# Kernel optimization log

Measured on AMD Instinct MI355X. Metric: run time of the kernel, lower is better.

The kernel has to match this reference:

```python
import jax, jax.numpy as jnp
from jax import lax
import numpy as np

N, CIN, COUT, K, LAT, H = 8, 512, 512, 3, 512, 32
CINT = (CIN + COUT) // 2  # inter_channels
DN = ('NCHW', 'OIHW', 'NCHW')


def setup_inputs() -> dict:
    key = jax.random.key(0)
    ks = jax.random.split(key, 16)
    f = jax.random.normal
    return {
        'x': f(ks[0], (N, CIN, H, H), jnp.float32),
        'v': f(ks[1], (N, LAT), jnp.float32),
        'y': f(ks[2], (N, 3, H, H), jnp.float32),
        'noise1': f(ks[3], (N, 1, 2 * H, 2 * H), jnp.float32),
        'noise2': f(ks[4], (N, 1, 2 * H, 2 * H), jnp.float32),
        # Up_Mod_Conv: weight stored transposed -> [in, out, k, k]
        'up_w': f(ks[5], (CIN, CINT, K, K), jnp.float32) * 0.05,
        'up_b': f(ks[6], (CINT,), jnp.float32) * 0.05,
        'up_sw': f(ks[7], (LAT, CIN), jnp.float32) * 0.02,
        'up_sb': jnp.ones((CIN,), jnp.float32),
        # Modulated_Conv2d: weight [out, in, k, k]
        'c_w': f(ks[8], (COUT, CINT, K, K), jnp.float32) * 0.05,
        'c_b': f(ks[9], (COUT,), jnp.float32) * 0.05,
        'c_sw': f(ks[10], (LAT, CINT), jnp.float32) * 0.02,
        'c_sb': jnp.ones((CINT,), jnp.float32),
        # toRGB: 1x1, no demodulation
        'rgb_w': f(ks[11], (3, COUT, 1, 1), jnp.float32) * 0.05,
        'rgb_b': f(ks[12], (3,), jnp.float32) * 0.05,
        'rgb_sw': f(ks[13], (LAT, COUT), jnp.float32) * 0.02,
        'rgb_sb': jnp.ones((COUT,), jnp.float32),
        'noise_strength': jnp.full((1,), 0.1, jnp.float32),
    }


def _lrelu(x):
    return jnp.where(x > 0, x, 0.2 * x)  # LeakyReLU(0.2)


def _mod_conv(x, v, W, b, sw, sb, demod, pad):
    # Per-sample modulation s_i * W; since conv is linear this equals
    # conv(x * s) followed by per-sample/out-channel demod division.
    s = v @ sw + sb  # [N, Cin]
    out = lax.conv_general_dilated(x * s[:, :, None, None], W, (1, 1),
                                   ((pad, pad), (pad, pad)), dimension_numbers=DN)
    if demod:
        # sigma_no = sqrt(sum_{i,h,w} (s_ni * W_oihw)^2 + eps)
        sigma = jnp.sqrt(jnp.einsum('oihw,ni->no', W * W, s * s) + 1e-8)
        out = out / sigma[:, :, None, None]
    return out + b[None, :, None, None]


def _up_mod_conv(x, v, W, b, sw, sb):
    s = v @ sw + sb  # [N, Cin]
    Wt = jnp.flip(W, axis=(2, 3)).transpose(1, 0, 2, 3)  # [out, in, k, k]
    out = lax.conv_general_dilated(x * s[:, :, None, None], Wt, (1, 1),
                                   ((1, 2), (1, 2)), lhs_dilation=(2, 2),
                                   dimension_numbers=DN)
    # demod sums over in-channel dim and spatial dims of [in,out,k,k] weight
    sigma = jnp.sqrt(jnp.einsum('iohw,ni->no', W * W, s * s) + 1e-8)
    return out / sigma[:, :, None, None] + b[None, :, None, None]


def reference(x, v, y, noise1, noise2, up_w, up_b, up_sw, up_sb,
              c_w, c_b, c_sw, c_sb, rgb_w, rgb_b, rgb_sw, rgb_sb,
              noise_strength):
    h = _up_mod_conv(x, v, up_w, up_b, up_sw, up_sb)          # [N, CINT, 2H, 2H]
    h = _lrelu(h + noise_strength[0] * noise1)
    h = _mod_conv(h, v, c_w, c_b, c_sw, c_sb, True, K // 2)   # [N, COUT, 2H, 2H]
    h = _lrelu(h + noise_strength[0] * noise2)
    rgb = _lrelu(_mod_conv(h, v, rgb_w, rgb_b, rgb_sw, rgb_sb, False, 0))
    y_up = jax.image.resize(y, (y.shape[0], y.shape[1], 2 * y.shape[2], 2 * y.shape[3]),
                            method='bilinear')  # matches torch align_corners=False
    return (h, y_up + rgb)
```

## Files before the change

kernel.cpp:

```cpp
#include <hip/hip_runtime.h>
#include <hip/hip_bf16.h>

typedef unsigned short u16;
typedef u16  u16x4 __attribute__((ext_vector_type(4)));
typedef __bf16 bf16;
typedef bf16 bf16x8 __attribute__((ext_vector_type(8)));
typedef float f32x4 __attribute__((ext_vector_type(4)));

__device__ __forceinline__ float b2f(u16 u){ return __uint_as_float(((unsigned)u)<<16); }
__device__ __forceinline__ u16 f2b(float f){ bf16 h = (bf16)f; return __builtin_bit_cast(u16, h); }
__device__ __forceinline__ float lrelu(float v){ return v > 0.f ? v : 0.2f*v; }

__device__ __forceinline__ void gll16(const u16* g, u16* l){
  __builtin_amdgcn_global_load_lds(
    (const __attribute__((address_space(1))) unsigned int*)(const void*)g,
    (__attribute__((address_space(3))) unsigned int*)(void*)l, 16, 0, 0);
}
#define VMCNT0() asm volatile("s_waitcnt vmcnt(0)" ::: "memory")
#define BAR()    { asm volatile("" ::: "memory"); __builtin_amdgcn_s_barrier(); asm volatile("" ::: "memory"); }


__global__ __launch_bounds__(256) void prep_w_up(const float* __restrict__ up_w,
                                                 u16* __restrict__ Wup_t, float* __restrict__ wsq_up){
  const int t = blockIdx.x*256 + threadIdx.x;
  const int i = t & 511, o = t >> 9;
  const float* src = up_w + ((i<<9) + o)*9;
  float sq = 0.f;
  #pragma unroll
  for (int ky=0; ky<3; ++ky)
    #pragma unroll
    for (int kx=0; kx<3; ++kx){
      float w = src[ky*3+kx];
      sq += w*w;
      Wup_t[ (((2-ky)*3 + (2-kx))<<18) + (o<<9) + i ] = f2b(w);
    }
  wsq_up[(o<<9)+i] = sq;
}

__global__ __launch_bounds__(256) void prep_w_c(const float* __restrict__ c_w,
                                                u16* __restrict__ Wc_t, float* __restrict__ wsq_c){
  const int t = blockIdx.x*256 + threadIdx.x;
  const int i = t & 511, o = t >> 9;
  const float* src = c_w + ((o<<9) + i)*9;
  float sq = 0.f;
  #pragma unroll
  for (int tap=0; tap<9; ++tap){
    float w = src[tap];
    sq += w*w;
    Wc_t[ (tap<<18) + (o<<9) + i ] = f2b(w);
  }
  wsq_c[(o<<9)+i] = sq;
}

__global__ __launch_bounds__(256) void prep_s(const float* __restrict__ v,
    const float* __restrict__ up_sw, const float* __restrict__ up_sb,
    const float* __restrict__ c_sw,  const float* __restrict__ c_sb,
    const float* __restrict__ rgb_sw,const float* __restrict__ rgb_sb,
    float* __restrict__ s_up, float* __restrict__ s_c, float* __restrict__ s_rgb){
  const int t = blockIdx.x*256 + threadIdx.x;
  const int j = t & 511, n = t >> 9;
  const float* vn = v + (n<<9);
  float a=0.f, b=0.f, c=0.f;
  for (int l=0; l<512; ++l){
    float vl = vn[l];
    a += vl*up_sw[(l<<9)+j];
    b += vl*c_sw[(l<<9)+j];
    c += vl*rgb_sw[(l<<9)+j];
  }
  s_up[t] = a + up_sb[j];
  s_c[t]  = b + c_sb[j];
  s_rgb[t]= c + rgb_sb[j];
}

__global__ __launch_bounds__(256) void prep_sigma(const float* __restrict__ wsq_up, const float* __restrict__ wsq_c,
    const float* __restrict__ s_up, const float* __restrict__ s_c,
    float* __restrict__ sinv_up, float* __restrict__ sinv_c){
  const int t = blockIdx.x*256 + threadIdx.x;
  const int o = t & 511, n = t >> 9;
  const float* su = s_up + (n<<9);
  const float* sc = s_c  + (n<<9);
  const float* wu = wsq_up + (o<<9);
  const float* wc = wsq_c  + (o<<9);
  float au=0.f, ac=0.f;
  for (int l=0; l<512; ++l){
    float s1 = su[l]; au += wu[l]*s1*s1;
    float s2 = sc[l]; ac += wc[l]*s2*s2;
  }
  sinv_up[t] = 1.f/sqrtf(au + 1e-8f);
  sinv_c[t]  = 1.f/sqrtf(ac + 1e-8f);
}

__global__ __launch_bounds__(256) void fill_xp(const float* __restrict__ x,
    const float* __restrict__ s_up, u16* __restrict__ xp){
  const int t = blockIdx.x*256 + threadIdx.x;
  const int q4 = (t&7)<<2;
  const int p  = (t>>3)&31;
  const int chn= t>>8;
  const int n  = chn>>9, ch = chn&511;
  const float s = s_up[chn];
  const float4 vx = *(const float4*)&x[ (((chn<<5)+p)<<5) + q4 ];
  const int base = (((n*33 + p)*36) + q4)<<9;
  xp[base +        ch] = f2b(vx.x*s);
  xp[base +  512 + ch] = f2b(vx.y*s);
  xp[base + 1024 + ch] = f2b(vx.z*s);
  xp[base + 1536 + ch] = f2b(vx.w*s);
}

__global__ __launch_bounds__(256, 2) void up_conv_k(
    const u16* __restrict__ xp, const u16* __restrict__ Wup_t,
    const float* __restrict__ sinv_up, const float* __restrict__ up_b,
    const float* __restrict__ s_c, const float* __restrict__ noise1,
    const float* __restrict__ nstr, u16* __restrict__ h1s)
{
  __shared__ __align__(16) u16 Bp[11520];
  __shared__ __align__(16) u16 Aa[8192];
  const int bid = blockIdx.x;
  const int og = bid & 3, tile = (bid>>2)&7, cls = (bid>>5)&3, n = bid>>7;
  const int cy = cls>>1, cx = cls&1;
  const int o0 = og<<7, r0 = tile<<2;
  const int tid = threadIdx.x;
  const int lane = tid & 63, wave = tid>>6;
  const int l15 = lane & 15, l4 = lane>>4;
  const int wm = wave>>1, wn = wave&1;
  const int xsw = l15 & 7;
  const int wub = tid & ~63;

  int wtap[4], dpl[4], dql[4]; int nt=0;
  for (int a = cy?0:1; a <= (cy?2:1); a += (cy?2:1))
    for (int b = cx?0:1; b <= (cx?2:1); b += (cx?2:1)){
      wtap[nt] = a*3+b; dpl[nt] = (cy+a-1)>>1; dql[nt] = (cx+b-1)>>1; ++nt;
    }

  f32x4 acc[4][4];
  #pragma unroll
  for (int i2=0;i2<4;++i2)
    #pragma unroll
    for (int j2=0;j2<4;++j2){ f32x4 z = {0.f,0.f,0.f,0.f}; acc[i2][j2]=z; }

  #pragma unroll 1
  for (int ci=0; ci<8; ++ci){
    const int i0 = ci<<6;
    BAR();
    #pragma unroll
    for (int k=0;k<6;++k){
      const int q = (k<<8) + tid;
      if (q < 1440){
        const int cell = q>>3, pc = q&7;
        const int rowl = cell/36, col = cell - rowl*36;
        const int cl = pc ^ (col&7);
        const u16* src = xp + (((n*33 + r0 + rowl)*36 + col)<<9) + i0 + (cl<<3);
        gll16(src, Bp + (((k<<8)+wub)<<3));
      }
    }
    #pragma unroll 1
    for (int t=0; t<nt; ++t){
      const int dp = dpl[t], dq = dql[t];
      #pragma unroll
      for (int k=0;k<4;++k){
        const int q = (k<<8) + tid;
        const int o = q>>3, pc = q&7;
        const int cl = pc ^ (o&7);
        const u16* src = Wup_t + (wtap[t]<<18) + ((o0+o)<<9) + i0 + (cl<<3);
        gll16(src, Aa + (((k<<8)+wub)<<3));
      }
      VMCNT0();
      BAR();
      bf16x8 af[4][2], bfr[4][2];
      #pragma unroll
      for (int fm=0; fm<4; ++fm){
        const int o_r = (wm<<6)+(fm<<4)+l15;
        #pragma unroll
        for (int kh=0; kh<2; ++kh)
          af[fm][kh] = *(const bf16x8*)&Aa[ (((o_r<<3) + (((kh<<2)+l4) ^ xsw))<<3) ];
      }
      #pragma unroll
      for (int fn=0; fn<4; ++fn){
        const int rr = (wn<<1) + (fn>>1), c = ((fn&1)<<4) + l15;
        const int row = rr + dp, col = c + dq;
        const int cell = row*36 + col, csw = col & 7;
        #pragma unroll
        for (int kh=0; kh<2; ++kh)
          bfr[fn][kh] = *(const bf16x8*)&Bp[ (((cell<<3) + (((kh<<2)+l4) ^ csw))<<3) ];
      }
      #pragma unroll
      for (int kh=0; kh<2; ++kh)
        #pragma unroll
        for (int fm=0; fm<4; ++fm)
          #pragma unroll
          for (int fn=0; fn<4; ++fn)
            acc[fm][fn] = __builtin_amdgcn_mfma_f32_16x16x32_bf16(af[fm][kh], bfr[fn][kh], acc[fm][fn], 0,0,0);
      BAR();
    }
  }
  const float ns = nstr[0];
  #pragma unroll
  for (int fm=0; fm<4; ++fm){
    const int oo0 = o0 + (wm<<6) + (fm<<4) + (l4<<2);
    float si[4], bb[4], sc2[4];
    #pragma unroll
    for (int r=0;r<4;++r){
      si[r] = sinv_up[(n<<9)+oo0+r];
      bb[r] = up_b[oo0+r];
      sc2[r]= s_c[(n<<9)+oo0+r];
    }
    #pragma unroll
    for (int fn=0; fn<4; ++fn){
      const int rr = (wn<<1) + (fn>>1), c = ((fn&1)<<4) + l15;
      const int Y = ((r0+rr)<<1) + cy, X = (c<<1) + cx;
      const float nz = ns * noise1[(n<<12) + (Y<<6) + X];
      u16x4 pk;
      #pragma unroll
      for (int r=0;r<4;++r){
        float v2 = acc[fm][fn][r]*si[r] + bb[r] + nz;
        pk[r] = f2b(lrelu(v2) * sc2[r]);
      }
      *(u16x4*)&h1s[ (((n*66 + Y+1)*66 + (X+1))<<9) + oo0 ] = pk;
    }
  }
}

__global__ __launch_bounds__(256, 2) void conv3x3_k(
    const u16* __restrict__ h1s, const u16* __restrict__ Wc_t,
    const float* __restrict__ sinv_c, const float* __restrict__ c_b,
    const float* __restrict__ noise2, const float* __restrict__ nstr,
    float* __restrict__ outh)
{
  __shared__ __align__(16) u16 Bp[16896];
  __shared__ __align__(16) u16 Aa[8192];
  const int bid = blockIdx.x;
  const int og = bid & 3, yp = (bid>>2)&31, n = bid>>7;
  const int o0 = og<<7, y0 = yp<<1;
  const int tid = threadIdx.x;
  const int lane = tid & 63, wave = tid>>6;
  const int l15 = lane & 15, l4 = lane>>4;
  const int wm = wave>>1, wn = wave&1;
  const int xsw = l15 & 7;
  const int wub = tid & ~63;

  f32x4 acc[4][4];
  #pragma unroll
  for (int i2=0;i2<4;++i2)
    #pragma unroll
    for (int j2=0;j2<4;++j2){ f32x4 z = {0.f,0.f,0.f,0.f}; acc[i2][j2]=z; }

  #pragma unroll 1
  for (int ci=0; ci<8; ++ci){
    const int i0 = ci<<6;
    BAR();
    #pragma unroll
    for (int k=0;k<9;++k){
      if (k==8 && tid>=64) continue;
      const int q = (k<<8) + tid;
      const int cell = q>>3, pc = q&7;
      const int row = cell/66, col = cell - row*66;
      const int cl = pc ^ (col&7);
      const u16* src = h1s + (((n*66 + y0 + row)*66 + col)<<9) + i0 + (cl<<3);
      gll16(src, Bp + (((k<<8)+wub)<<3));
    }
    #pragma unroll 1
    for (int tap=0; tap<9; ++tap){
      const int ky = tap/3, kx = tap - ky*3;
      #pragma unroll
      for (int k=0;k<4;++k){
        const int q = (k<<8) + tid;
        const int o = q>>3, pc = q&7;
        const int cl = pc ^ (o&7);
        const u16* src = Wc_t + (tap<<18) + ((o0+o)<<9) + i0 + (cl<<3);
        gll16(src, Aa + (((k<<8)+wub)<<3));
      }
      VMCNT0();
      BAR();
      bf16x8 af[4][2], bfr[4][2];
      #pragma unroll
      for (int fm=0; fm<4; ++fm){
        const int o_r = (wm<<6)+(fm<<4)+l15;
        #pragma unroll
        for (int kh=0; kh<2; ++kh)
          af[fm][kh] = *(const bf16x8*)&Aa[ (((o_r<<3) + (((kh<<2)+l4) ^ xsw))<<3) ];
      }
      #pragma unroll
      for (int fn=0; fn<4; ++fn){
        const int colx = (fn<<4) + l15 + kx;
        const int cell = (wn + ky)*66 + colx, csw = colx & 7;
        #pragma unroll
        for (int kh=0; kh<2; ++kh)
          bfr[fn][kh] = *(const bf16x8*)&Bp[ (((cell<<3) + (((kh<<2)+l4) ^ csw))<<3) ];
      }
      #pragma unroll
      for (int kh=0; kh<2; ++kh)
        #pragma unroll
        for (int fm=0; fm<4; ++fm)
          #pragma unroll
          for (int fn=0; fn<4; ++fn)
            acc[fm][fn] = __builtin_amdgcn_mfma_f32_16x16x32_bf16(af[fm][kh], bfr[fn][kh], acc[fm][fn], 0,0,0);
      BAR();
    }
  }
  const float ns = nstr[0];
  #pragma unroll
  for (int fm=0; fm<4; ++fm){
    #pragma unroll
    for (int r=0;r<4;++r){
      const int oo = o0 + (wm<<6)+(fm<<4)+(l4<<2)+r;
      const float si = sinv_c[(n<<9)+oo], bb = c_b[oo];
      #pragma unroll
      for (int fn=0; fn<4; ++fn){
        const int xq = (fn<<4)+l15;
        const int Y = y0 + wn;
        float v2 = acc[fm][fn][r]*si + bb + ns*noise2[(n<<12)+(Y<<6)+xq];
        outh[ (((n<<9)+oo)<<12) + (Y<<6) + xq ] = lrelu(v2);
      }
    }
  }
}

__global__ __launch_bounds__(256) void rgb_k(const float* __restrict__ h2,
    const float* __restrict__ s_rgb, const float* __restrict__ rgb_w, const float* __restrict__ rgb_b,
    const float* __restrict__ yin, float* __restrict__ out1)
{
  __shared__ float coef[3][512];
  __shared__ float part[4][3][64];
  const int n = blockIdx.x>>6, Y = blockIdx.x&63;
  const int tid = threadIdx.x;
  for (int t = tid; t < 1536; t += 256){
    int c = t>>9, o = t&511;
    coef[c][o] = rgb_w[(c<<9)+o]*s_rgb[(n<<9)+o];
  }
  __syncthreads();
  const int wave = tid>>6, lane = tid&63;
  const float* base = h2 + ((size_t)(n<<9))*4096 + (Y<<6) + lane;
  float a0=0.f,a1=0.f,a2=0.f;
  for (int e=0;e<128;++e){
    int o = (wave<<7)+e;
    float h = base[(size_t)o<<12];
    a0 += h*coef[0][o]; a1 += h*coef[1][o]; a2 += h*coef[2][o];
  }
  part[wave][0][lane]=a0; part[wave][1][lane]=a1; part[wave][2][lane]=a2;
  __syncthreads();
  if (tid < 192){
    const int c = tid>>6, x2 = tid&63;
    float s = part[0][c][x2]+part[1][c][x2]+part[2][c][x2]+part[3][c][x2] + rgb_b[c];
    s = lrelu(s);
    float fy = 0.5f*Y - 0.25f, fx = 0.5f*x2 - 0.25f;
    int y0i = (int)floorf(fy); float wy = fy - y0i;
    int x0i = (int)floorf(fx); float wx = fx - x0i;
    int y0c = y0i<0?0:y0i, y1c = y0i+1>31?31:y0i+1;
    int x0c = x0i<0?0:x0i, x1c = x0i+1>31?31:x0i+1;
    const float* yb = yin + ((n*3 + c)<<10);
    float v00 = yb[(y0c<<5)+x0c], v01 = yb[(y0c<<5)+x1c];
    float v10 = yb[(y1c<<5)+x0c], v11 = yb[(y1c<<5)+x1c];
    float yup = (1.f-wy)*((1.f-wx)*v00 + wx*v01) + wy*((1.f-wx)*v10 + wx*v11);
    out1[ (((n*3+c)<<12)) + (Y<<6) + x2 ] = yup + s;
  }
}

extern "C" void kernel_launch(void* const* d_in, const int* in_sizes, int n_in,
                              void* d_out, int out_size, void* d_ws, size_t ws_size,
                              hipStream_t stream) {
  const float* x      = (const float*)d_in[0];
  const float* v      = (const float*)d_in[1];
  const float* yin    = (const float*)d_in[2];
  const float* noise1 = (const float*)d_in[3];
  const float* noise2 = (const float*)d_in[4];
  const float* up_w   = (const float*)d_in[5];
  const float* up_b   = (const float*)d_in[6];
  const float* up_sw  = (const float*)d_in[7];
  const float* up_sb  = (const float*)d_in[8];
  const float* c_w    = (const float*)d_in[9];
  const float* c_b    = (const float*)d_in[10];
  const float* c_sw   = (const float*)d_in[11];
  const float* c_sb   = (const float*)d_in[12];
  const float* rgb_w  = (const float*)d_in[13];
  const float* rgb_b  = (const float*)d_in[14];
  const float* rgb_sw = (const float*)d_in[15];
  const float* rgb_sb = (const float*)d_in[16];
  const float* nstr   = (const float*)d_in[17];

  char* w = (char*)d_ws;
  u16*   Wup_t  = (u16*)(w);
  u16*   Wc_t   = (u16*)(w + 4718592);
  float* wsq_up = (float*)(w + 9437184);
  float* wsq_c  = (float*)(w + 10485760);
  float* s_up   = (float*)(w + 11534336);
  float* s_c    = (float*)(w + 11550720);
  float* s_rgb  = (float*)(w + 11567104);
  float* sinv_up= (float*)(w + 11583488);
  float* sinv_c = (float*)(w + 11599872);
  u16*   xp     = (u16*)(w + 11616256);
  u16*   h1s    = (u16*)(w + 21348352);

  float* outh = (float*)d_out;
  float* out1 = (float*)d_out + 16777216;

  hipMemsetAsync(xp,  0, 9732096,  stream);
  hipMemsetAsync(h1s, 0, 35684352, stream);

  prep_w_up <<<1024, 256, 0, stream>>>(up_w, Wup_t, wsq_up);
  prep_w_c  <<<1024, 256, 0, stream>>>(c_w,  Wc_t,  wsq_c);
  prep_s    <<<16,   256, 0, stream>>>(v, up_sw, up_sb, c_sw, c_sb, rgb_sw, rgb_sb, s_up, s_c, s_rgb);
  prep_sigma<<<16,   256, 0, stream>>>(wsq_up, wsq_c, s_up, s_c, sinv_up, sinv_c);
  fill_xp   <<<4096, 256, 0, stream>>>(x, s_up, xp);
  up_conv_k <<<1024, 256, 0, stream>>>(xp, Wup_t, sinv_up, up_b, s_c, noise1, nstr, h1s);
  conv3x3_k <<<1024, 256, 0, stream>>>(h1s, Wc_t, sinv_c, c_b, noise2, nstr, outh);
  rgb_k     <<<512,  256, 0, stream>>>(outh, s_rgb, rgb_w, rgb_b, yin, out1);
}
```

Baseline: 484.9 us.

## Double-buffer weight tiles, remap blocks across XCDs, vectorize xp fill

Both conv kernels now double-buffer the per-tap weight tile in LDS. The next tap's weights are prefetched while the current tap's MFMAs run, waiting with vmcnt(4) instead of draining all loads. MFMA sections are wrapped in s_setprio. Block indices in the conv and rgb kernels are permuted so neighbouring work lands on the same XCD for L2 reuse. fill_xp is rewritten to write 16-byte channel-contiguous packets instead of scattered 2-byte stores, and LDS use per block grows, which may limit occupancy.

```diff
diff --git a/kernel.cpp b/kernel.cpp
--- a/kernel.cpp
+++ b/kernel.cpp
@@ -3,6 +3,7 @@
 
 typedef unsigned short u16;
 typedef u16  u16x4 __attribute__((ext_vector_type(4)));
+typedef u16  u16x8 __attribute__((ext_vector_type(8)));
 typedef __bf16 bf16;
 typedef bf16 bf16x8 __attribute__((ext_vector_type(8)));
 typedef float f32x4 __attribute__((ext_vector_type(4)));
@@ -17,6 +18,7 @@
     (__attribute__((address_space(3))) unsigned int*)(void*)l, 16, 0, 0);
 }
 #define VMCNT0() asm volatile("s_waitcnt vmcnt(0)" ::: "memory")
+#define VMCNT4() asm volatile("s_waitcnt vmcnt(4)" ::: "memory")
 #define BAR()    { asm volatile("" ::: "memory"); __builtin_amdgcn_s_barrier(); asm volatile("" ::: "memory"); }
 
 
@@ -92,18 +94,22 @@
 
 __global__ __launch_bounds__(256) void fill_xp(const float* __restrict__ x,
     const float* __restrict__ s_up, u16* __restrict__ xp){
-  const int t = blockIdx.x*256 + threadIdx.x;
-  const int q4 = (t&7)<<2;
-  const int p  = (t>>3)&31;
-  const int chn= t>>8;
-  const int n  = chn>>9, ch = chn&511;
-  const float s = s_up[chn];
-  const float4 vx = *(const float4*)&x[ (((chn<<5)+p)<<5) + q4 ];
-  const int base = (((n*33 + p)*36) + q4)<<9;
-  xp[base +        ch] = f2b(vx.x*s);
-  xp[base +  512 + ch] = f2b(vx.y*s);
-  xp[base + 1024 + ch] = f2b(vx.z*s);
-  xp[base + 1536 + ch] = f2b(vx.w*s);
+  const int b = blockIdx.x;
+  const int n = b>>5, p = b&31;
+  const int t = threadIdx.x;
+  const int q = t&31, g = t>>5;
+  const int cb = g<<6;
+  #pragma unroll
+  for (int j=0;j<8;++j){
+    const int ch0 = cb + (j<<3);
+    u16x8 pk;
+    #pragma unroll
+    for (int e=0;e<8;++e){
+      float vv = x[ (((n<<9)+ch0+e)<<10) + (p<<5) + q ] * s_up[(n<<9)+ch0+e];
+      pk[e] = f2b(vv);
+    }
+    *(u16x8*)&xp[ (((n*33+p)*36 + q)<<9) + ch0 ] = pk;
+  }
 }
 
 __global__ __launch_bounds__(256, 2) void up_conv_k(
@@ -113,8 +119,9 @@
     const float* __restrict__ nstr, u16* __restrict__ h1s)
 {
   __shared__ __align__(16) u16 Bp[11520];
-  __shared__ __align__(16) u16 Aa[8192];
-  const int bid = blockIdx.x;
+  __shared__ __align__(16) u16 Aa[2][8192];
+  const int braw = blockIdx.x;
+  const int bid = ((braw&7)<<7) | (braw>>3);
   const int og = bid & 3, tile = (bid>>2)&7, cls = (bid>>5)&3, n = bid>>7;
   const int cy = cls>>1, cx = cls&1;
   const int o0 = og<<7, r0 = tile<<2;
@@ -140,7 +147,6 @@
   #pragma unroll 1
   for (int ci=0; ci<8; ++ci){
     const int i0 = ci<<6;
-    BAR();
     #pragma unroll
     for (int k=0;k<6;++k){
       const int q = (k<<8) + tid;
@@ -148,22 +154,38 @@
         const int cell = q>>3, pc = q&7;
         const int rowl = cell/36, col = cell - rowl*36;
         const int cl = pc ^ (col&7);
-        const u16* src = xp + (((n*33 + r0 + rowl)*36 + col)<<9) + i0 + (cl<<3);
-        gll16(src, Bp + (((k<<8)+wub)<<3));
-      }
-    }
+        gll16(xp + (((n*33 + r0 + rowl)*36 + col)<<9) + i0 + (cl<<3),
+              Bp + (((k<<8)+wub)<<3));
+      }
+    }
+    #pragma unroll
+    for (int k=0;k<4;++k){
+      const int q = (k<<8) + tid;
+      const int o = q>>3, pc = q&7;
+      const int cl = pc ^ (o&7);
+      gll16(Wup_t + (wtap[0]<<18) + ((o0+o)<<9) + i0 + (cl<<3),
+            &Aa[0][ (((k<<8)+wub)<<3) ]);
+    }
+    VMCNT0();
+    BAR();
     #pragma unroll 1
     for (int t=0; t<nt; ++t){
       const int dp = dpl[t], dq = dql[t];
-      #pragma unroll
-      for (int k=0;k<4;++k){
-        const int q = (k<<8) + tid;
-        const int o = q>>3, pc = q&7;
-        const int cl = pc ^ (o&7);
-        const u16* src = Wup_t + (wtap[t]<<18) + ((o0+o)<<9) + i0 + (cl<<3);
-        gll16(src, Aa + (((k<<8)+wub)<<3));
-      }
-      VMCNT0();
+      const int cur = t & 1;
+      if (t+1 < nt){
+        const int nxt = (t+1)&1;
+        #pragma unroll
+        for (int k=0;k<4;++k){
+          const int q = (k<<8) + tid;
+          const int o = q>>3, pc = q&7;
+          const int cl = pc ^ (o&7);
+          gll16(Wup_t + (wtap[t+1]<<18) + ((o0+o)<<9) + i0 + (cl<<3),
+                &Aa[nxt][ (((k<<8)+wub)<<3) ]);
+        }
+        VMCNT4();
+      } else {
+        VMCNT0();
+      }
       BAR();
       bf16x8 af[4][2], bfr[4][2];
       #pragma unroll
@@ -171,7 +193,7 @@
         const int o_r = (wm<<6)+(fm<<4)+l15;
         #pragma unroll
         for (int kh=0; kh<2; ++kh)
-          af[fm][kh] = *(const bf16x8*)&Aa[ (((o_r<<3) + (((kh<<2)+l4) ^ xsw))<<3) ];
+          af[fm][kh] = *(const bf16x8*)&Aa[cur][ (((o_r<<3) + (((kh<<2)+l4) ^ xsw))<<3) ];
       }
       #pragma unroll
       for (int fn=0; fn<4; ++fn){
@@ -182,6 +204,7 @@
         for (int kh=0; kh<2; ++kh)
           bfr[fn][kh] = *(const bf16x8*)&Bp[ (((cell<<3) + (((kh<<2)+l4) ^ csw))<<3) ];
       }
+      __builtin_amdgcn_s_setprio(1);
       #pragma unroll
       for (int kh=0; kh<2; ++kh)
         #pragma unroll
@@ -189,6 +212,7 @@
           #pragma unroll
           for (int fn=0; fn<4; ++fn)
             acc[fm][fn] = __builtin_amdgcn_mfma_f32_16x16x32_bf16(af[fm][kh], bfr[fn][kh], acc[fm][fn], 0,0,0);
+      __builtin_amdgcn_s_setprio(0);
       BAR();
     }
   }
@@ -226,8 +250,9 @@
     float* __restrict__ outh)
 {
   __shared__ __align__(16) u16 Bp[16896];
-  __shared__ __align__(16) u16 Aa[8192];
-  const int bid = blockIdx.x;
+  __shared__ __align__(16) u16 Aa[2][8192];
+  const int braw = blockIdx.x;
+  const int bid = ((braw&7)<<7) | (braw>>3);
   const int og = bid & 3, yp = (bid>>2)&31, n = bid>>7;
   const int o0 = og<<7, y0 = yp<<1;
   const int tid = threadIdx.x;
@@ -246,7 +271,6 @@
   #pragma unroll 1
   for (int ci=0; ci<8; ++ci){
     const int i0 = ci<<6;
-    BAR();
     #pragma unroll
     for (int k=0;k<9;++k){
       if (k==8 && tid>=64) continue;
@@ -254,21 +278,37 @@
       const int cell = q>>3, pc = q&7;
       const int row = cell/66, col = cell - row*66;
       const int cl = pc ^ (col&7);
-      const u16* src = h1s + (((n*66 + y0 + row)*66 + col)<<9) + i0 + (cl<<3);
-      gll16(src, Bp + (((k<<8)+wub)<<3));
-    }
+      gll16(h1s + (((n*66 + y0 + row)*66 + col)<<9) + i0 + (cl<<3),
+            Bp + (((k<<8)+wub)<<3));
+    }
+    #pragma unroll
+    for (int k=0;k<4;++k){
+      const int q = (k<<8) + tid;
+      const int o = q>>3, pc = q&7;
+      const int cl = pc ^ (o&7);
+      gll16(Wc_t + ((o0+o)<<9) + i0 + (cl<<3),
+            &Aa[0][ (((k<<8)+wub)<<3) ]);
+    }
+    VMCNT0();
+    BAR();
     #pragma unroll 1
     for (int tap=0; tap<9; ++tap){
       const int ky = tap/3, kx = tap - ky*3;
-      #pragma unroll
-      for (int k=0;k<4;++k){
-        const int q = (k<<8) + tid;
-        const int o = q>>3, pc = q&7;
-        const int cl = pc ^ (o&7);
-        const u16* src = Wc_t + (tap<<18) + ((o0+o)<<9) + i0 + (cl<<3);
-        gll16(src, Aa + (((k<<8)+wub)<<3));
-      }
-      VMCNT0();
+      const int cur = tap & 1;
+      if (tap < 8){
+        const int nxt = (tap+1)&1;
+        #pragma unroll
+        for (int k=0;k<4;++k){
+          const int q = (k<<8) + tid;
+          const int o = q>>3, pc = q&7;
+          const int cl = pc ^ (o&7);
+          gll16(Wc_t + ((tap+1)<<18) + ((o0+o)<<9) + i0 + (cl<<3),
+                &Aa[nxt][ (((k<<8)+wub)<<3) ]);
+        }
+        VMCNT4();
+      } else {
+        VMCNT0();
+      }
       BAR();
       bf16x8 af[4][2], bfr[4][2];
       #pragma unroll
@@ -276,7 +316,7 @@
         const int o_r = (wm<<6)+(fm<<4)+l15;
         #pragma unroll
         for (int kh=0; kh<2; ++kh)
-          af[fm][kh] = *(const bf16x8*)&Aa[ (((o_r<<3) + (((kh<<2)+l4) ^ xsw))<<3) ];
+          af[fm][kh] = *(const bf16x8*)&Aa[cur][ (((o_r<<3) + (((kh<<2)+l4) ^ xsw))<<3) ];
       }
       #pragma unroll
       for (int fn=0; fn<4; ++fn){
@@ -286,6 +326,7 @@
         for (int kh=0; kh<2; ++kh)
           bfr[fn][kh] = *(const bf16x8*)&Bp[ (((cell<<3) + (((kh<<2)+l4) ^ csw))<<3) ];
       }
+      __builtin_amdgcn_s_setprio(1);
       #pragma unroll
       for (int kh=0; kh<2; ++kh)
         #pragma unroll
@@ -293,6 +334,7 @@
           #pragma unroll
           for (int fn=0; fn<4; ++fn)
             acc[fm][fn] = __builtin_amdgcn_mfma_f32_16x16x32_bf16(af[fm][kh], bfr[fn][kh], acc[fm][fn], 0,0,0);
+      __builtin_amdgcn_s_setprio(0);
       BAR();
     }
   }
@@ -320,7 +362,9 @@
 {
   __shared__ float coef[3][512];
   __shared__ float part[4][3][64];
-  const int n = blockIdx.x>>6, Y = blockIdx.x&63;
+  const int braw = blockIdx.x;
+  const int sb = ((braw&7)<<6) | (braw>>3);
+  const int n = sb>>6, Y = sb&63;
   const int tid = threadIdx.x;
   for (int t = tid; t < 1536; t += 256){
     int c = t>>9, o = t&511;
@@ -399,7 +443,7 @@
   prep_w_c  <<<1024, 256, 0, stream>>>(c_w,  Wc_t,  wsq_c);
   prep_s    <<<16,   256, 0, stream>>>(v, up_sw, up_sb, c_sw, c_sb, rgb_sw, rgb_sb, s_up, s_c, s_rgb);
   prep_sigma<<<16,   256, 0, stream>>>(wsq_up, wsq_c, s_up, s_c, sinv_up, sinv_c);
-  fill_xp   <<<4096, 256, 0, stream>>>(x, s_up, xp);
+  fill_xp   <<<256,  256, 0, stream>>>(x, s_up, xp);
   up_conv_k <<<1024, 256, 0, stream>>>(xp, Wup_t, sinv_up, up_b, s_c, noise1, nstr, h1s);
   conv3x3_k <<<1024, 256, 0, stream>>>(h1s, Wc_t, sinv_c, c_b, noise2, nstr, outh);
   rgb_k     <<<512,  256, 0, stream>>>(outh, s_rgb, rgb_w, rgb_b, yin, out1);
```

Measured after the change: 436.3 us. 1.11x faster.
